# Kernel optimization log

Hardware: AMD Instinct MI355X
Metric: run time of the kernel (lower is better)

Reference implementation:

```python
import jax, jax.numpy as jnp
import numpy as np

EPS = 1e-5
NEG_SLOPE = 0.2


def _minmax(a):
    m = jnp.min(a)
    return (a - m) / (jnp.max(a) - m)


def _bn(x2d, gamma, beta):
    # train-mode BatchNorm1d: stats over axis 0 (biased variance)
    mu = x2d.mean(0)
    var = x2d.var(0)
    return gamma * (x2d - mu) * jax.lax.rsqrt(var + EPS) + beta


def _leaky(a):
    return jnp.where(a >= 0, a, NEG_SLOPE * a)


def setup_inputs() -> dict:
    key = jax.random.key(0)
    ks = jax.random.split(key, 10)
    B, C, N = 256, 1024, 80
    stdv = 1.0 / np.sqrt(C)
    return {
        "x": jax.random.normal(ks[0], (B, C, N), jnp.float32),
        "out1": jax.random.normal(ks[1], (B, N), jnp.float32),
        "adj_param": jax.random.uniform(ks[2], (N, N), jnp.float32),
        "static_weight": jax.random.uniform(ks[3], (C, C), jnp.float32, -stdv, stdv),
        "dynamic_weight": jax.random.uniform(ks[4], (C, C), jnp.float32, -stdv, stdv),
        "conv_global_w": jax.random.normal(ks[5], (C, C), jnp.float32) * 0.02,
        "conv_global_b": jnp.zeros((C,), jnp.float32),
        "conv_co_w": jax.random.normal(ks[6], (N, 2 * C), jnp.float32) * 0.02,
        "conv_co_b": jnp.zeros((N,), jnp.float32),
        "bn_gamma": jnp.ones((C,), jnp.float32),
        "bn_beta": jnp.zeros((C,), jnp.float32),
        "bng_gamma": jnp.ones((C,), jnp.float32),
        "bng_beta": jnp.zeros((C,), jnp.float32),
    }


def reference(x, out1, adj_param, static_weight, dynamic_weight,
              conv_global_w, conv_global_b, conv_co_w, conv_co_b,
              bn_gamma, bn_beta, bng_gamma, bng_beta):
    B, C, N = x.shape

    # ---- static GCN ----
    sadj = _minmax(adj_param)                               # (N,N)
    D = jax.lax.rsqrt(sadj.sum(1))                          # A.sum(1)^-0.5
    adj = D[:, None] * sadj.T * D[None, :]                  # gen_adj, diag matmuls as broadcast
    support = jnp.einsum('bcn,co->bno', x, static_weight)   # (B,N,C)
    h = jnp.einsum('nm,bmo->bno', adj, support)             # (B,N,C)
    h = _bn(h.reshape(-1, C), bn_gamma, bn_beta).reshape(B, N, C)
    out_static = _leaky(h).transpose(0, 2, 1)               # (B,C,N)
    x2 = x + out_static

    # ---- dynamic graph construction ----
    glb = x2.mean(2)                                        # GAP over nodes -> (B,C)
    glb = glb @ conv_global_w.T + conv_global_b             # 1x1 conv
    glb = _leaky(_bn(glb, bng_gamma, bng_beta))             # BN over batch (L=1)
    cat = jnp.concatenate([jnp.broadcast_to(glb[:, :, None], (B, C, N)), x2], axis=1)  # (B,2C,N)
    dadj = jnp.einsum('oc,bcn->bon', conv_co_w, cat) + conv_co_b[None, :, None]        # (B,N,N)
    dadj = _minmax(dadj)

    # ---- adjacency loss ----
    t1 = jnp.einsum('bn,bnm->bm', out1, dadj) / N
    loss = jnp.sum(jnp.linalg.norm(out1 - t1, axis=1))
    loss = loss + jnp.sum(jnp.linalg.norm((dadj - sadj).reshape(B, -1), axis=1))

    # ---- dynamic GCN ----
    Dd = jax.lax.rsqrt(dadj.sum(2))                         # (B,N)
    tadj = Dd[:, :, None] * dadj.transpose(0, 2, 1) * Dd[:, None, :]
    sup = jnp.einsum('bcn,co->bno', x2, dynamic_weight)
    h2 = jnp.einsum('bnm,bmo->bno', tadj, sup)
    h2 = _bn(h2.reshape(-1, C), bn_gamma, bn_beta).reshape(B, N, C).transpose(0, 2, 1)
    h2 = _leaky(h2)                                         # (B,C,N)
    return h2, loss
```

## Files before the change

kernel.cpp:

```cpp
#include <hip/hip_runtime.h>
#include <hip/hip_bf16.h>
#include <math.h>

#define TPB 256

constexpr int   B_  = 256;
constexpr int   C_  = 1024;
constexpr int   N_  = 80;
constexpr int   BNr = B_ * N_;
constexpr int   CN  = C_ * N_;
constexpr long  BCN = (long)B_ * C_ * N_;
constexpr int   NN  = N_ * N_;
constexpr int   BNN = B_ * NN;
constexpr float EPSf = 1e-5f;

typedef __bf16 bf16x8 __attribute__((ext_vector_type(8)));
typedef float  f32x4  __attribute__((ext_vector_type(4)));

__device__ __forceinline__ float leakyf(float v) { return v >= 0.0f ? v : 0.2f * v; }

__device__ __forceinline__ ushort f2bf(float f) {
  __hip_bfloat16 h = __float2bfloat16(f);
  ushort u; __builtin_memcpy(&u, &h, 2); return u;
}
__device__ __forceinline__ float b2f(ushort u) {
  __hip_bfloat16 h; __builtin_memcpy(&h, &u, 2);
  return __bfloat162float(h);
}

#define GLOBAL_AS __attribute__((address_space(1)))
#define LDS_AS    __attribute__((address_space(3)))
__device__ __forceinline__ void load_lds16(const void* g, void* l) {
  __builtin_amdgcn_global_load_lds((const GLOBAL_AS void*)g, (LDS_AS void*)l, 16, 0, 0);
}

__global__ void k_prep_adj(const float* __restrict__ ap, float* __restrict__ sadj,
                           ushort* __restrict__ adj_bf, float* __restrict__ lossa) {
  __shared__ float s[NN];
  __shared__ float red[TPB];
  __shared__ float s_lo, s_hi;
  __shared__ float sD[N_];
  const int t = threadIdx.x;
  float lo = 3.4e38f, hi = -3.4e38f;
  for (int i = t; i < NN; i += TPB) { float v = ap[i]; s[i] = v; lo = fminf(lo, v); hi = fmaxf(hi, v); }
  red[t] = lo; __syncthreads();
  for (int o = 128; o > 0; o >>= 1) { if (t < o) red[t] = fminf(red[t], red[t + o]); __syncthreads(); }
  if (t == 0) s_lo = red[0];
  __syncthreads();
  red[t] = hi; __syncthreads();
  for (int o = 128; o > 0; o >>= 1) { if (t < o) red[t] = fmaxf(red[t], red[t + o]); __syncthreads(); }
  if (t == 0) s_hi = red[0];
  __syncthreads();
  const float inv = 1.0f / (s_hi - s_lo);
  for (int i = t; i < NN; i += TPB) { float v = (s[i] - s_lo) * inv; s[i] = v; sadj[i] = v; }
  __syncthreads();
  if (t < N_) { float sum = 0.f; for (int m = 0; m < N_; ++m) sum += s[t * N_ + m]; sD[t] = rsqrtf(sum); }
  if (t == 0) *lossa = 0.0f;
  __syncthreads();
  for (int i = t; i < N_ * 96; i += TPB) {
    const int n = i / 96, m = i % 96;
    adj_bf[i] = f2bf((m < N_) ? sD[n] * s[m * N_ + n] * sD[m] : 0.0f);
  }
}

__global__ void k_w_bf_t(const float* __restrict__ W, ushort* __restrict__ Wt) {
  __shared__ float s[32][33];
  const int t = threadIdx.x;
  const int tx = t % 32, ty = t / 32;
  const int r0 = blockIdx.y * 32, c0 = blockIdx.x * 32;
#pragma unroll
  for (int k = 0; k < 4; ++k) s[ty + 8 * k][tx] = W[(size_t)(r0 + ty + 8 * k) * C_ + c0 + tx];
  __syncthreads();
#pragma unroll
  for (int k = 0; k < 4; ++k) Wt[(size_t)(c0 + ty + 8 * k) * C_ + r0 + tx] = f2bf(s[tx][ty + 8 * k]);
}

__global__ void k_wco_bf(const float* __restrict__ Wco, ushort* __restrict__ Wco1t,
                         ushort* __restrict__ Wco2t) {
  const int i4 = (blockIdx.x * TPB + threadIdx.x) * 4;
  const int o = i4 >> 11, k = i4 & 2047;
  float4 v = *(const float4*)&Wco[(size_t)o * 2048 + k];
  ushort4 u;
  u.x = f2bf(v.x); u.y = f2bf(v.y); u.z = f2bf(v.z); u.w = f2bf(v.w);
  if (k < C_) *(ushort4*)&Wco1t[(size_t)o * C_ + k] = u;
  else        *(ushort4*)&Wco2t[(size_t)o * C_ + (k - C_)] = u;
}

__global__ void k_cvt_bf(const float* __restrict__ W, ushort* __restrict__ Wb) {
  const long i4 = ((long)blockIdx.x * TPB + threadIdx.x) * 4;
  float4 v = *(const float4*)&W[i4];
  ushort4 u;
  u.x = f2bf(v.x); u.y = f2bf(v.y); u.z = f2bf(v.z); u.w = f2bf(v.w);
  *(ushort4*)&Wb[i4] = u;
}

__global__ void k_zero_go(float* __restrict__ go) {
  const int i = (blockIdx.x * TPB + threadIdx.x) * 4;
  float4 z = make_float4(0.f, 0.f, 0.f, 0.f);
  *(float4*)&go[i] = z;
}

__global__ __launch_bounds__(256) void k_fold_mfma(const float* __restrict__ Xf32,
                                                   const ushort* __restrict__ Xbf,
                                                   const void* __restrict__ adjsrc,
                                                   ushort* __restrict__ outp, int mode,
                                                   const float* __restrict__ dmm) {
  __shared__ __align__(16) ushort sX[128][104];
  __shared__ __align__(16) ushort sAdj[80][104];
  __shared__ float sD[N_];
  const int t = threadIdx.x;
  const int b  = blockIdx.x >> 3;
  const int c0 = (blockIdx.x & 7) * 128;

  if (mode == 0) {
    const ushort* ab = (const ushort*)adjsrc;
    for (int i = t; i < (N_ * 96) / 4; i += TPB) {
      ushort4 v = *(const ushort4*)&ab[i * 4];
      *(ushort4*)&sAdj[(i * 4) / 96][(i * 4) % 96] = v;
    }
    __syncthreads();
  } else {
    float* sF = (float*)&sX[0][0];
    const float* db = (const float*)adjsrc + (size_t)b * NN;
    const float lo = dmm[0], inv = dmm[1];
    for (int i = t; i < NN / 4; i += TPB) {
      float4 v = *(const float4*)&db[i * 4];
      v.x = (v.x - lo) * inv; v.y = (v.y - lo) * inv;
      v.z = (v.z - lo) * inv; v.w = (v.w - lo) * inv;
      *(float4*)&sF[i * 4] = v;
    }
    __syncthreads();
    if (t < N_) { float s = 0.f; for (int m = 0; m < N_; ++m) s += sF[t * N_ + m]; sD[t] = rsqrtf(s); }
    __syncthreads();
    for (int i = t; i < N_ * 96; i += TPB) {
      const int n = i / 96, m = i % 96;
      sAdj[n][m] = f2bf((m < N_) ? sF[m * N_ + n] * sD[n] * sD[m] : 0.0f);
    }
    __syncthreads();
  }

  if (mode == 0) {
    const float* Xb = Xf32 + ((size_t)b * C_ + c0) * N_;
    for (int i = t; i < (128 * N_) / 4; i += TPB) {
      float4 v = *(const float4*)&Xb[i * 4];
      const int r = (i * 4) / N_, m = (i * 4) % N_;
      ushort4 u; u.x = f2bf(v.x); u.y = f2bf(v.y); u.z = f2bf(v.z); u.w = f2bf(v.w);
      *(ushort4*)&sX[r][m] = u;
    }
  } else {
    const ushort* Xb = Xbf + ((size_t)b * C_ + c0) * N_;
    for (int i = t; i < (128 * N_) / 8; i += TPB) {
      const int r = i / 10, m = (i % 10) * 8;
      uint4 v = *(const uint4*)&Xb[(size_t)r * N_ + m];
      *(uint4*)&sX[r][m] = v;
    }
  }
  for (int i = t; i < (128 * 16) / 4; i += TPB) {
    const int r = i / 4, m = 80 + (i % 4) * 4;
    ushort4 z; z.x = 0; z.y = 0; z.z = 0; z.w = 0;
    *(ushort4*)&sX[r][m] = z;
  }
  __syncthreads();

  const int lane = t & 63, wid = t >> 6;
  const int l16 = lane & 15, lq = lane >> 4;
  f32x4 acc[2][5];
#pragma unroll
  for (int i = 0; i < 2; ++i)
#pragma unroll
    for (int j = 0; j < 5; ++j) { f32x4 z = {0.f, 0.f, 0.f, 0.f}; acc[i][j] = z; }
  bf16x8 af[2][3], bfr[5][3];
#pragma unroll
  for (int i = 0; i < 2; ++i)
#pragma unroll
    for (int kk = 0; kk < 3; ++kk)
      af[i][kk] = *(const bf16x8*)&sX[wid * 32 + i * 16 + l16][kk * 32 + lq * 8];
#pragma unroll
  for (int j = 0; j < 5; ++j)
#pragma unroll
    for (int kk = 0; kk < 3; ++kk)
      bfr[j][kk] = *(const bf16x8*)&sAdj[j * 16 + l16][kk * 32 + lq * 8];
#pragma unroll
  for (int i = 0; i < 2; ++i)
#pragma unroll
    for (int j = 0; j < 5; ++j)
#pragma unroll
      for (int kk = 0; kk < 3; ++kk)
        acc[i][j] = __builtin_amdgcn_mfma_f32_16x16x32_bf16(af[i][kk], bfr[j][kk], acc[i][j], 0, 0, 0);

  ushort* ob = outp + (size_t)b * CN;
#pragma unroll
  for (int i = 0; i < 2; ++i) {
    const int c = c0 + wid * 32 + i * 16 + lq * 4;
#pragma unroll
    for (int j = 0; j < 5; ++j) {
      const int n = j * 16 + l16;
      ushort4 u;
      u.x = f2bf(acc[i][j][0]); u.y = f2bf(acc[i][j][1]);
      u.z = f2bf(acc[i][j][2]); u.w = f2bf(acc[i][j][3]);
      *(ushort4*)&ob[(size_t)n * C_ + c] = u;
    }
  }
}

__global__ __launch_bounds__(512, 2) void k_gemm_256(const ushort* __restrict__ A,
                                                     const ushort* __restrict__ Bt,
                                                     void* __restrict__ outp, int out_bf) {
  __shared__ ushort sA[2][256 * 64];
  __shared__ ushort sB[2][256 * 64];
  const int t = threadIdx.x;
  const int lane = t & 63, wid = t >> 6;
  const int wm = wid >> 2, wn = wid & 3;
  const int l16 = lane & 15, lq = lane >> 4;

  const int lin = blockIdx.x;
  const int xcd = lin & 7, bi = lin >> 3;
  const int tm = xcd * 10 + (bi >> 2);
  const int tn = bi & 3;
  const int m0 = tm * 256, o0 = tn * 256;

  const int srow = t >> 3;
  const int sswz = ((t & 7) ^ ((t >> 3) & 7)) * 8;

  f32x4 acc[8][4];
#pragma unroll
  for (int i = 0; i < 8; ++i)
#pragma unroll
    for (int j = 0; j < 4; ++j) { f32x4 z = {0.f, 0.f, 0.f, 0.f}; acc[i][j] = z; }

  bf16x8 afr[4][2], bfr0[2][2], bfr1[2][2];

#define STA(PAR, ROWB, KT) load_lds16(A  + (size_t)(m0 + (ROWB) + srow) * C_ + (KT) * 64 + sswz, \
                                      &sA[PAR][((ROWB) + (wid << 3)) * 64])
#define STB(PAR, ROWB, KT) load_lds16(Bt + (size_t)(o0 + (ROWB) + srow) * C_ + (KT) * 64 + sswz, \
                                      &sB[PAR][((ROWB) + (wid << 3)) * 64])
#define STA_H(PAR, H, KT) { STA(PAR, (H)*128, KT); STA(PAR, (H)*128 + 64, KT); }
#define STB_H(PAR, H, KT) { STB(PAR, (H)*128, KT); STB(PAR, (H)*128 + 64, KT); }

#define RDA(PAR, MH)                                                                      \
  _Pragma("unroll") for (int fi = 0; fi < 4; ++fi) {                                      \
    const int row = ((MH) ? 128 : 0) + wm * 64 + fi * 16 + l16;                           \
    _Pragma("unroll") for (int kk = 0; kk < 2; ++kk)                                      \
      afr[fi][kk] = *(const bf16x8*)&sA[PAR][row * 64 + ((kk * 4 + lq) ^ (l16 & 7)) * 8]; \
  }
#define RDB(PAR, NH, DST)                                                                 \
  _Pragma("unroll") for (int gi = 0; gi < 2; ++gi) {                                      \
    const int row = ((NH) ? 128 : 0) + wn * 32 + gi * 16 + l16;                           \
    _Pragma("unroll") for (int kk = 0; kk < 2; ++kk)                                      \
      DST[gi][kk] = *(const bf16x8*)&sB[PAR][row * 64 + ((kk * 4 + lq) ^ (l16 & 7)) * 8]; \
  }

#define MFMAS(MH, NH, BF)                                                          \
  _Pragma("unroll") for (int kk = 0; kk < 2; ++kk)                                 \
  _Pragma("unroll") for (int fi = 0; fi < 4; ++fi)                                 \
  _Pragma("unroll") for (int gi = 0; gi < 2; ++gi)                                 \
    acc[(MH) * 4 + fi][(NH) * 2 + gi] = __builtin_amdgcn_mfma_f32_16x16x32_bf16(   \
        afr[fi][kk], BF[gi][kk], acc[(MH) * 4 + fi][(NH) * 2 + gi], 0, 0, 0);

#define PHASE(MH, NH, BF, RD, STAGES, VMW)                                         \
  {                                                                                \
    RD                                                                             \
    STAGES                                                                         \
    asm volatile("s_barrier" ::: "memory");                                        \
    asm volatile("s_waitcnt lgkmcnt(0)" ::: "memory");                             \
    __builtin_amdgcn_s_setprio(1);                                                 \
    MFMAS(MH, NH, BF)                                                              \
    __builtin_amdgcn_s_setprio(0);                                                 \
    VMW                                                                            \
    asm volatile("s_barrier" ::: "memory");                                        \
  }

  STA_H(0, 0, 0); STA_H(0, 1, 0); STB_H(0, 0, 0); STB_H(0, 1, 0);
  STA_H(1, 0, 1); STB_H(1, 1, 1);
  asm volatile("s_waitcnt vmcnt(4)" ::: "memory");
  asm volatile("s_barrier" ::: "memory");

  for (int i = 0; i < 7; ++i) {
    const int t1 = 2 * i + 1, t2 = 2 * i + 2, t3 = 2 * i + 3;
    PHASE(0, 0, bfr0, RDA(0, 0) RDB(0, 0, bfr0), { STA_H(1, 1, t1); }, {})
    PHASE(0, 1, bfr1, RDB(0, 1, bfr1),           { STB_H(1, 0, t1); }, {})
    PHASE(1, 1, bfr1, RDA(0, 1),                 { STA_H(0, 0, t2); }, {})
    PHASE(1, 0, bfr0, {},                        { STB_H(0, 1, t2); }, { asm volatile("s_waitcnt vmcnt(4)" ::: "memory"); })
    PHASE(0, 0, bfr0, RDA(1, 0) RDB(1, 0, bfr0), { STA_H(0, 1, t2); }, {})
    PHASE(0, 1, bfr1, RDB(1, 1, bfr1),           { STB_H(0, 0, t2); }, {})
    PHASE(1, 1, bfr1, RDA(1, 1),                 { STA_H(1, 0, t3); }, {})
    PHASE(1, 0, bfr0, {},                        { STB_H(1, 1, t3); }, { asm volatile("s_waitcnt vmcnt(4)" ::: "memory"); })
  }
  PHASE(0, 0, bfr0, RDA(0, 0) RDB(0, 0, bfr0), { STA_H(1, 1, 15); }, {})
  PHASE(0, 1, bfr1, RDB(0, 1, bfr1),           { STB_H(1, 0, 15); }, {})
  PHASE(1, 1, bfr1, RDA(0, 1),                 {}, {})
  PHASE(1, 0, bfr0, {},                        {}, { asm volatile("s_waitcnt vmcnt(0)" ::: "memory"); })
  PHASE(0, 0, bfr0, RDA(1, 0) RDB(1, 0, bfr0), {}, {})
  PHASE(0, 1, bfr1, RDB(1, 1, bfr1),           {}, {})
  PHASE(1, 1, bfr1, RDA(1, 1),                 {}, {})
  PHASE(1, 0, bfr0, {},                        {}, {})

#pragma unroll
  for (int f = 0; f < 8; ++f) {
    const int gmb = (f < 4) ? (wm * 64 + f * 16) : (128 + wm * 64 + (f - 4) * 16);
    const int mg = m0 + gmb + lq * 4;
    const int b  = mg / 80;
    const int n0 = mg - b * 80;
#pragma unroll
    for (int gi = 0; gi < 4; ++gi) {
      const int gnb = (gi < 2) ? (wn * 32 + gi * 16) : (128 + wn * 32 + (gi - 2) * 16);
      const int og = o0 + gnb + l16;
      const size_t off = (size_t)b * CN + (size_t)og * N_ + n0;
      if (out_bf) {
        ushort4 u;
        u.x = f2bf(acc[f][gi][0]); u.y = f2bf(acc[f][gi][1]);
        u.z = f2bf(acc[f][gi][2]); u.w = f2bf(acc[f][gi][3]);
        *(ushort4*)((ushort*)outp + off) = u;
      } else {
        *(f32x4*)((float*)outp + off) = acc[f][gi];
      }
    }
  }
#undef STA
#undef STB
#undef STA_H
#undef STB_H
#undef RDA
#undef RDB
#undef MFMAS
#undef PHASE
}

__global__ __launch_bounds__(256) void k_dadj_mfma(const ushort* __restrict__ A,
                                                   const ushort* __restrict__ Bw,
                                                   const float* __restrict__ go,
                                                   const float* __restrict__ bco,
                                                   float* __restrict__ dadj,
                                                   float* __restrict__ bmin,
                                                   float* __restrict__ bmax) {
  __shared__ ushort smA[128 * 32];
  __shared__ ushort smB[80 * 32];
  const int t = threadIdx.x;
  const int lane = t & 63, wid = t >> 6;
  const int m0 = blockIdx.x * 128;
  const int rto = t >> 2, ch = t & 3;
  const size_t gA0 = (size_t)(m0 + rto) * C_ + (size_t)ch * 8;
  ushort* ldsA = smA + wid * 512;
  const int l16 = lane & 15, lq = lane >> 4;
  const int wrow = wid * 32;
  f32x4 zero = {0.f, 0.f, 0.f, 0.f};
  f32x4 acc[2][5];
#pragma unroll
  for (int i = 0; i < 2; ++i)
#pragma unroll
    for (int j = 0; j < 5; ++j) acc[i][j] = zero;
  for (int k0 = 0; k0 < C_; k0 += 32) {
    load_lds16(A + gA0 + k0,            ldsA);
    load_lds16(A + gA0 + 64 * C_ + k0,  ldsA + 2048);
    {
      const int idx = t;
      uint4 v = *(const uint4*)&Bw[(size_t)(idx >> 2) * C_ + k0 + (idx & 3) * 8];
      *(uint4*)&smB[idx * 8] = v;
      if (t < 64) {
        const int idx2 = 256 + t;
        uint4 v2 = *(const uint4*)&Bw[(size_t)(idx2 >> 2) * C_ + k0 + (idx2 & 3) * 8];
        *(uint4*)&smB[idx2 * 8] = v2;
      }
    }
    __syncthreads();
    bf16x8 af[2], bfr[5];
#pragma unroll
    for (int i = 0; i < 2; ++i) af[i]  = *(const bf16x8*)&smA[(wrow + i * 16 + l16) * 32 + lq * 8];
#pragma unroll
    for (int j = 0; j < 5; ++j) bfr[j] = *(const bf16x8*)&smB[(j * 16 + l16) * 32 + lq * 8];
#pragma unroll
    for (int i = 0; i < 2; ++i)
#pragma unroll
      for (int j = 0; j < 5; ++j)
        acc[i][j] = __builtin_amdgcn_mfma_f32_16x16x32_bf16(af[i], bfr[j], acc[i][j], 0, 0, 0);
    __syncthreads();
  }
  float vlo = 3.4e38f, vhi = -3.4e38f;
#pragma unroll
  for (int i = 0; i < 2; ++i) {
    const int mg = m0 + wrow + i * 16 + lq * 4;
    const int b  = mg / 80;
    const int n0 = mg - b * 80;
    const float* gob = go + b * N_;
#pragma unroll
    for (int j = 0; j < 5; ++j) {
      const int o = j * 16 + l16;
      const float g = gob[o] + bco[o];
      f32x4 v = acc[i][j];
      v[0] += g; v[1] += g; v[2] += g; v[3] += g;
      vlo = fminf(vlo, fminf(fminf(v[0], v[1]), fminf(v[2], v[3])));
      vhi = fmaxf(vhi, fmaxf(fmaxf(v[0], v[1]), fmaxf(v[2], v[3])));
      *(f32x4*)&dadj[(size_t)b * NN + (size_t)o * N_ + n0] = v;
    }
  }
  float* red = (float*)smA;
  red[t] = vlo; red[TPB + t] = vhi;
  __syncthreads();
  for (int o = 128; o > 0; o >>= 1) {
    if (t < o) {
      red[t] = fminf(red[t], red[t + o]);
      red[TPB + t] = fmaxf(red[TPB + t], red[TPB + t + o]);
    }
    __syncthreads();
  }
  if (t == 0) { bmin[blockIdx.x] = red[0]; bmax[blockIdx.x] = red[TPB]; }
}

__global__ __launch_bounds__(256) void k_glb_mfma(const ushort* __restrict__ A,
                                                  const ushort* __restrict__ Bw,
                                                  const float* __restrict__ bias,
                                                  float* __restrict__ outp) {
  __shared__ ushort smA[2][64 * 32];
  __shared__ ushort smB[2][64 * 32];
  const int t = threadIdx.x;
  const int lane = t & 63, wid = t >> 6;
  const int o0 = blockIdx.x * 64, m0 = blockIdx.y * 64;
  const int rto = t >> 2, ch = t & 3;
  const size_t gA0 = (size_t)(m0 + rto) * C_ + (size_t)ch * 8;
  const size_t gB0 = (size_t)(o0 + rto) * C_ + (size_t)ch * 8;
  const int l16 = lane & 15, lq = lane >> 4;
  const int wm = wid & 1, wn = wid >> 1;
  f32x4 zero = {0.f, 0.f, 0.f, 0.f};
  f32x4 acc[2][2];
#pragma unroll
  for (int i = 0; i < 2; ++i)
#pragma unroll
    for (int j = 0; j < 2; ++j) acc[i][j] = zero;
  for (int k0 = 0; k0 < C_; k0 += 64) {
    load_lds16(A  + gA0 + k0,       smA[0] + wid * 512);
    load_lds16(A  + gA0 + k0 + 32,  smA[1] + wid * 512);
    load_lds16(Bw + gB0 + k0,       smB[0] + wid * 512);
    load_lds16(Bw + gB0 + k0 + 32,  smB[1] + wid * 512);
    __syncthreads();
#pragma unroll
    for (int h = 0; h < 2; ++h) {
      bf16x8 af[2], bfr[2];
#pragma unroll
      for (int i = 0; i < 2; ++i) af[i]  = *(const bf16x8*)&smA[h][(wm * 32 + i * 16 + l16) * 32 + lq * 8];
#pragma unroll
      for (int j = 0; j < 2; ++j) bfr[j] = *(const bf16x8*)&smB[h][(wn * 32 + j * 16 + l16) * 32 + lq * 8];
#pragma unroll
      for (int i = 0; i < 2; ++i)
#pragma unroll
        for (int j = 0; j < 2; ++j)
          acc[i][j] = __builtin_amdgcn_mfma_f32_16x16x32_bf16(af[i], bfr[j], acc[i][j], 0, 0, 0);
    }
    __syncthreads();
  }
#pragma unroll
  for (int i = 0; i < 2; ++i) {
    const int mg = m0 + wm * 32 + i * 16 + lq * 4;
#pragma unroll
    for (int j = 0; j < 2; ++j) {
      const int og = o0 + wn * 32 + j * 16 + l16;
      const float bs = bias[og];
      f32x4 v = acc[i][j];
#pragma unroll
      for (int r = 0; r < 4; ++r) outp[(size_t)(mg + r) * C_ + og] = v[r] + bs;
    }
  }
}

__global__ __launch_bounds__(256) void k_go_mfma(const ushort* __restrict__ A,
                                                 const ushort* __restrict__ Bw,
                                                 float* __restrict__ go) {
  __shared__ ushort smA[128 * 32];
  __shared__ ushort smB[80 * 32];
  const int t = threadIdx.x;
  const int lane = t & 63, wid = t >> 6;
  const int kbase = blockIdx.x * 128;
  const int m0 = blockIdx.y * 128;
  const int rto = t >> 2, ch = t & 3;
  const size_t gA0 = (size_t)(m0 + rto) * C_ + (size_t)ch * 8;
  ushort* ldsA = smA + wid * 512;
  const int l16 = lane & 15, lq = lane >> 4;
  const int wrow = wid * 32;
  f32x4 zero = {0.f, 0.f, 0.f, 0.f};
  f32x4 acc[2][5];
#pragma unroll
  for (int i = 0; i < 2; ++i)
#pragma unroll
    for (int j = 0; j < 5; ++j) acc[i][j] = zero;
  for (int kk0 = 0; kk0 < 128; kk0 += 32) {
    const int k0 = kbase + kk0;
    load_lds16(A + gA0 + k0,            ldsA);
    load_lds16(A + gA0 + 64 * C_ + k0,  ldsA + 2048);
    {
      const int idx = t;
      uint4 v = *(const uint4*)&Bw[(size_t)(idx >> 2) * C_ + k0 + (idx & 3) * 8];
      *(uint4*)&smB[idx * 8] = v;
      if (t < 64) {
        const int idx2 = 256 + t;
        uint4 v2 = *(const uint4*)&Bw[(size_t)(idx2 >> 2) * C_ + k0 + (idx2 & 3) * 8];
        *(uint4*)&smB[idx2 * 8] = v2;
      }
    }
    __syncthreads();
    bf16x8 af[2], bfr[5];
#pragma unroll
    for (int i = 0; i < 2; ++i) af[i]  = *(const bf16x8*)&smA[(wrow + i * 16 + l16) * 32 + lq * 8];
#pragma unroll
    for (int j = 0; j < 5; ++j) bfr[j] = *(const bf16x8*)&smB[(j * 16 + l16) * 32 + lq * 8];
#pragma unroll
    for (int i = 0; i < 2; ++i)
#pragma unroll
      for (int j = 0; j < 5; ++j)
        acc[i][j] = __builtin_amdgcn_mfma_f32_16x16x32_bf16(af[i], bfr[j], acc[i][j], 0, 0, 0);
    __syncthreads();
  }
#pragma unroll
  for (int i = 0; i < 2; ++i) {
    const int mg = m0 + wrow + i * 16 + lq * 4;
#pragma unroll
    for (int j = 0; j < 5; ++j) {
      const int o = j * 16 + l16;
#pragma unroll
      for (int r = 0; r < 4; ++r)
        atomicAdd(&go[(size_t)(mg + r) * N_ + o], acc[i][j][r]);
    }
  }
}

__global__ void k_bn_stats_bf(const ushort* __restrict__ X, float* __restrict__ mu, float* __restrict__ rstd) {
  const int c = blockIdx.x, t = threadIdx.x;
  const ushort* base = X + (long)c * N_;
  float s = 0.f, sq = 0.f;
  for (int i4 = t; i4 < BNr / 4; i4 += TPB) {
    const int b = i4 / 20, n0 = (i4 % 20) * 4;
    ushort4 v = *(const ushort4*)&base[(long)b * CN + n0];
    const float f0 = b2f(v.x), f1 = b2f(v.y), f2 = b2f(v.z), f3 = b2f(v.w);
    s += f0 + f1 + f2 + f3;
    sq += f0 * f0 + f1 * f1 + f2 * f2 + f3 * f3;
  }
  __shared__ float rs[TPB], rq[TPB];
  rs[t] = s; rq[t] = sq; __syncthreads();
  for (int o = 128; o > 0; o >>= 1) { if (t < o) { rs[t] += rs[t + o]; rq[t] += rq[t + o]; } __syncthreads(); }
  if (t == 0) {
    const float m = rs[0] / BNr;
    const float var = rq[0] / BNr - m * m;
    mu[c] = m;
    rstd[c] = rsqrtf(var + EPSf);
  }
}

__global__ __launch_bounds__(256) void k_x2_fused(
    const float* __restrict__ x, ushort* __restrict__ hx,
    const float* __restrict__ g, const float* __restrict__ be,
    const float* __restrict__ mu, const float* __restrict__ rstd,
    ushort* __restrict__ x2t, ushort* __restrict__ glb0b) {
  __shared__ float s[64][84];
  __shared__ float pg[64], pm[64], pb[64];
  const int t = threadIdx.x;
  const long row0 = (long)blockIdx.x * 64;
  const int b = (int)(row0 >> 10), c0 = (int)(row0 & 1023);
  if (t < 64) {
    const int c = c0 + t;
    pg[t] = g[c] * rstd[c]; pm[t] = mu[c]; pb[t] = be[c];
  }
  __syncthreads();
  const float* xb = x  + row0 * N_;
  ushort*      hb = hx + row0 * N_;
  for (int i4 = t; i4 < (64 * N_) / 4; i4 += TPB) {
    const int e = i4 * 4, r = e / N_, n = e % N_;
    float4 xv = *(const float4*)&xb[e];
    ushort4 hu = *(const ushort4*)&hb[e];
    const float gm = pg[r], m = pm[r], bb = pb[r];
    float4 o;
    o.x = xv.x + leakyf(gm * (b2f(hu.x) - m) + bb);
    o.y = xv.y + leakyf(gm * (b2f(hu.y) - m) + bb);
    o.z = xv.z + leakyf(gm * (b2f(hu.z) - m) + bb);
    o.w = xv.w + leakyf(gm * (b2f(hu.w) - m) + bb);
    *(float4*)&s[r][n] = o;
    ushort4 ou;
    ou.x = f2bf(o.x); ou.y = f2bf(o.y); ou.z = f2bf(o.z); ou.w = f2bf(o.w);
    *(ushort4*)&hb[e] = ou;
  }
  __syncthreads();
  const int tx = t % 16, ty = t / 16;
  ushort* tb = x2t + (size_t)b * CN + c0 + tx * 4;
#pragma unroll
  for (int u = 0; u < 5; ++u) {
    const int n = ty + 16 * u;
    ushort4 v;
    v.x = f2bf(s[tx * 4 + 0][n]); v.y = f2bf(s[tx * 4 + 1][n]);
    v.z = f2bf(s[tx * 4 + 2][n]); v.w = f2bf(s[tx * 4 + 3][n]);
    *(ushort4*)&tb[(size_t)n * C_] = v;
  }
  {
    const int r = t >> 2, q = t & 3;
    float sacc = 0.f;
    for (int n = q; n < N_; n += 4) sacc += s[r][n];
    sacc += __shfl_down(sacc, 1);
    sacc += __shfl_down(sacc, 2);
    if (q == 0) glb0b[(size_t)b * C_ + c0 + r] = f2bf(sacc * (1.0f / N_));
  }
}

__global__ void k_bng(const float* __restrict__ glb1, const float* __restrict__ gg,
                      const float* __restrict__ gb, ushort* __restrict__ glbf) {
  const int c = blockIdx.x, t = threadIdx.x;
  const float v = glb1[(long)t * C_ + c];
  __shared__ float rs[TPB], rq[TPB];
  rs[t] = v; rq[t] = v * v; __syncthreads();
  for (int o = 128; o > 0; o >>= 1) { if (t < o) { rs[t] += rs[t + o]; rq[t] += rq[t + o]; } __syncthreads(); }
  __shared__ float sm, sr;
  if (t == 0) { const float m = rs[0] / B_; const float var = rq[0] / B_ - m * m; sm = m; sr = rsqrtf(var + EPSf); }
  __syncthreads();
  glbf[(long)t * C_ + c] = f2bf(leakyf(gg[c] * (v - sm) * sr + gb[c]));
}

__global__ void k_minmax2(const float* __restrict__ bmin, const float* __restrict__ bmax, float* __restrict__ dmm) {
  const int t = threadIdx.x;
  float lo = (t < 160) ? bmin[t] : 3.4e38f;
  float hi = (t < 160) ? bmax[t] : -3.4e38f;
  __shared__ float rl[TPB], rh[TPB];
  rl[t] = lo; rh[t] = hi; __syncthreads();
  for (int o = 128; o > 0; o >>= 1) { if (t < o) { rl[t] = fminf(rl[t], rl[t + o]); rh[t] = fmaxf(rh[t], rh[t + o]); } __syncthreads(); }
  if (t == 0) { dmm[0] = rl[0]; dmm[1] = 1.0f / (rh[0] - rl[0]); }
}

__global__ void k_loss(const float* __restrict__ dadj, const float* __restrict__ sadj,
                       const float* __restrict__ out1, float* __restrict__ lossa,
                       const float* __restrict__ dmm) {
  const int b = blockIdx.x, t = threadIdx.x;
  const float* db = dadj + (long)b * NN;
  const float* o1 = out1 + b * N_;
  const float lo = dmm[0], inv = dmm[1];
  float p2 = 0.f;
  for (int i = t; i < NN; i += TPB) { const float d = (db[i] - lo) * inv - sadj[i]; p2 += d * d; }
  float p1 = 0.f;
  if (t < N_) {
    float acc = 0.f;
    for (int n = 0; n < N_; ++n) acc += o1[n] * ((db[n * N_ + t] - lo) * inv);
    const float d = o1[t] - acc * (1.0f / N_);
    p1 = d * d;
  }
  __shared__ float red[TPB];
  __shared__ float s2;
  red[t] = p2; __syncthreads();
  for (int o = 128; o > 0; o >>= 1) { if (t < o) red[t] += red[t + o]; __syncthreads(); }
  if (t == 0) s2 = red[0];
  __syncthreads();
  red[t] = p1; __syncthreads();
  for (int o = 128; o > 0; o >>= 1) { if (t < o) red[t] += red[t + o]; __syncthreads(); }
  if (t == 0) atomicAdd(lossa, sqrtf(s2) + sqrtf(red[0]));
}

__global__ void k_final(const ushort* __restrict__ h2, float* __restrict__ outp,
                        const float* __restrict__ g, const float* __restrict__ be,
                        const float* __restrict__ mu, const float* __restrict__ rstd,
                        const float* __restrict__ lossa) {
  const long i = ((long)blockIdx.x * TPB + threadIdx.x) * 4;
  const int c = (int)((i / N_) % C_);
  ushort4 hu = *(const ushort4*)&h2[i];
  const float gm = g[c] * rstd[c], m = mu[c], bb = be[c];
  float4 v;
  v.x = leakyf(gm * (b2f(hu.x) - m) + bb);
  v.y = leakyf(gm * (b2f(hu.y) - m) + bb);
  v.z = leakyf(gm * (b2f(hu.z) - m) + bb);
  v.w = leakyf(gm * (b2f(hu.w) - m) + bb);
  *(float4*)&outp[i] = v;
  if (blockIdx.x == 0 && threadIdx.x == 0) outp[BCN] = *lossa;
}

extern "C" void kernel_launch(void* const* d_in, const int* in_sizes, int n_in,
                              void* d_out, int out_size, void* d_ws, size_t ws_size,
                              hipStream_t stream) {
  const float* x    = (const float*)d_in[0];
  const float* out1 = (const float*)d_in[1];
  const float* ap   = (const float*)d_in[2];
  const float* Ws   = (const float*)d_in[3];
  const float* Wd   = (const float*)d_in[4];
  const float* Wg   = (const float*)d_in[5];
  const float* bg   = (const float*)d_in[6];
  const float* Wco  = (const float*)d_in[7];
  const float* bco  = (const float*)d_in[8];
  const float* bn_g  = (const float*)d_in[9];
  const float* bn_b  = (const float*)d_in[10];
  const float* bng_g = (const float*)d_in[11];
  const float* bng_b = (const float*)d_in[12];
  float* out = (float*)d_out;

  float* w = (float*)d_ws;
  float* sadj  = w;
  float* dadj  = sadj + NN;
  float* glb0  = dadj + BNN;
  float* glb1  = glb0 + B_ * C_;
  float* glbf  = glb1 + B_ * C_;
  float* go    = glbf + B_ * C_;
  float* mu1   = go + BNr;
  float* rstd1 = mu1 + C_;
  float* mu2   = rstd1 + C_;
  float* rstd2 = mu2 + C_;
  float* bmin  = rstd2 + C_;
  float* bmax  = bmin + 512;
  float* dmm   = bmax + 512;
  float* lossa = dmm + 2;
  ushort* ub   = (ushort*)(((uintptr_t)(lossa + 1) + 255) & ~(uintptr_t)255);
  ushort* xa_bf  = ub;
  ushort* hT_bf  = xa_bf + BCN;
  ushort* Wts    = hT_bf + BCN;
  ushort* Wtd    = Wts + (size_t)C_ * C_;
  ushort* Wco2t  = Wtd + (size_t)C_ * C_;
  ushort* adj_bf = Wco2t + (size_t)N_ * C_;
  ushort* Wg_bf   = (ushort*)dadj;
  ushort* Wco1t   = (ushort*)dadj + (size_t)C_ * C_;
  ushort* glb0_bf = (ushort*)glb0;
  ushort* glbf_bf = (ushort*)glbf;
  ushort* x2t_bf  = xa_bf;

  k_prep_adj<<<1, TPB, 0, stream>>>(ap, sadj, adj_bf, lossa);
  k_w_bf_t<<<dim3(32, 32), TPB, 0, stream>>>(Ws, Wts);
  k_w_bf_t<<<dim3(32, 32), TPB, 0, stream>>>(Wd, Wtd);
  k_wco_bf<<<(N_ * 2 * C_) / (4 * TPB), TPB, 0, stream>>>(Wco, Wco1t, Wco2t);
  k_cvt_bf<<<(C_ * C_) / (4 * TPB), TPB, 0, stream>>>(Wg, Wg_bf);
  k_zero_go<<<BNr / (4 * TPB), TPB, 0, stream>>>(go);

  k_fold_mfma<<<B_ * 8, TPB, 0, stream>>>(x, hT_bf, adj_bf, xa_bf, 0, dmm);
  k_gemm_256<<<320, 512, 0, stream>>>(xa_bf, Wts, hT_bf, 1);
  k_bn_stats_bf<<<C_, TPB, 0, stream>>>(hT_bf, mu1, rstd1);
  k_x2_fused<<<(B_ * C_) / 64, TPB, 0, stream>>>(x, hT_bf, bn_g, bn_b, mu1, rstd1,
                                                 x2t_bf, glb0_bf);

  k_glb_mfma<<<dim3(C_ / 64, B_ / 64), TPB, 0, stream>>>(glb0_bf, Wg_bf, bg, glb1);
  k_bng<<<C_, TPB, 0, stream>>>(glb1, bng_g, bng_b, glbf_bf);
  k_go_mfma<<<dim3(8, B_ / 128), TPB, 0, stream>>>(glbf_bf, Wco1t, go);
  k_dadj_mfma<<<BNr / 128, TPB, 0, stream>>>(x2t_bf, Wco2t, go, bco, dadj, bmin, bmax);
  k_minmax2<<<1, TPB, 0, stream>>>(bmin, bmax, dmm);

  k_loss<<<B_, TPB, 0, stream>>>(dadj, sadj, out1, lossa, dmm);

  k_fold_mfma<<<B_ * 8, TPB, 0, stream>>>(x, hT_bf, dadj, xa_bf, 1, dmm);
  k_gemm_256<<<320, 512, 0, stream>>>(xa_bf, Wtd, hT_bf, 1);
  k_bn_stats_bf<<<C_, TPB, 0, stream>>>(hT_bf, mu2, rstd2);
  k_final<<<(int)(BCN / (4 * TPB)), TPB, 0, stream>>>(hT_bf, out, bn_g, bn_b, mu2, rstd2, lossa);
}
```

Baseline: 534.5 us.

## Fuse BN statistics into GEMM epilogue and merge prep kernels into one launch

Each GEMM block now reduces per-channel sum and sum-of-squares from its fp32 accumulators, combining them in LDS and then with global atomics. This removes the two separate BN-stats kernels that re-read the full bf16 hidden tensor. Consumers derive mean and rstd from these sums inline. The six weight-conversion, zeroing and adjacency-prep kernels are merged into one block-indexed launch, which also zeroes the new stat accumulators. In exchange, stats come from unrounded accumulators, the float atomics make summation order nondeterministic, and reusing the sA LDS buffer for the reduction may race with waves still reading it.

```diff
diff --git a/kernel.cpp b/kernel.cpp
--- a/kernel.cpp
+++ b/kernel.cpp
@@ -34,70 +34,72 @@
   __builtin_amdgcn_global_load_lds((const GLOBAL_AS void*)g, (LDS_AS void*)l, 16, 0, 0);
 }
 
-__global__ void k_prep_adj(const float* __restrict__ ap, float* __restrict__ sadj,
-                           ushort* __restrict__ adj_bf, float* __restrict__ lossa) {
-  __shared__ float s[NN];
+__global__ __launch_bounds__(256) void k_prep_all(
+    const float* __restrict__ Ws, const float* __restrict__ Wd,
+    const float* __restrict__ Wco, const float* __restrict__ Wg,
+    ushort* __restrict__ Wts, ushort* __restrict__ Wtd,
+    ushort* __restrict__ Wco1t, ushort* __restrict__ Wco2t, ushort* __restrict__ Wg_bf,
+    float* __restrict__ zbase,
+    const float* __restrict__ ap, float* __restrict__ sadj,
+    ushort* __restrict__ adj_bf, float* __restrict__ lossa) {
+  __shared__ float sh[NN];
   __shared__ float red[TPB];
+  __shared__ float sD[N_];
   __shared__ float s_lo, s_hi;
-  __shared__ float sD[N_];
   const int t = threadIdx.x;
-  float lo = 3.4e38f, hi = -3.4e38f;
-  for (int i = t; i < NN; i += TPB) { float v = ap[i]; s[i] = v; lo = fminf(lo, v); hi = fmaxf(hi, v); }
-  red[t] = lo; __syncthreads();
-  for (int o = 128; o > 0; o >>= 1) { if (t < o) red[t] = fminf(red[t], red[t + o]); __syncthreads(); }
-  if (t == 0) s_lo = red[0];
-  __syncthreads();
-  red[t] = hi; __syncthreads();
-  for (int o = 128; o > 0; o >>= 1) { if (t < o) red[t] = fmaxf(red[t], red[t + o]); __syncthreads(); }
-  if (t == 0) s_hi = red[0];
-  __syncthreads();
-  const float inv = 1.0f / (s_hi - s_lo);
-  for (int i = t; i < NN; i += TPB) { float v = (s[i] - s_lo) * inv; s[i] = v; sadj[i] = v; }
-  __syncthreads();
-  if (t < N_) { float sum = 0.f; for (int m = 0; m < N_; ++m) sum += s[t * N_ + m]; sD[t] = rsqrtf(sum); }
-  if (t == 0) *lossa = 0.0f;
-  __syncthreads();
-  for (int i = t; i < N_ * 96; i += TPB) {
-    const int n = i / 96, m = i % 96;
-    adj_bf[i] = f2bf((m < N_) ? sD[n] * s[m * N_ + n] * sD[m] : 0.0f);
-  }
-}
-
-__global__ void k_w_bf_t(const float* __restrict__ W, ushort* __restrict__ Wt) {
-  __shared__ float s[32][33];
-  const int t = threadIdx.x;
-  const int tx = t % 32, ty = t / 32;
-  const int r0 = blockIdx.y * 32, c0 = blockIdx.x * 32;
-#pragma unroll
-  for (int k = 0; k < 4; ++k) s[ty + 8 * k][tx] = W[(size_t)(r0 + ty + 8 * k) * C_ + c0 + tx];
-  __syncthreads();
-#pragma unroll
-  for (int k = 0; k < 4; ++k) Wt[(size_t)(c0 + ty + 8 * k) * C_ + r0 + tx] = f2bf(s[tx][ty + 8 * k]);
-}
-
-__global__ void k_wco_bf(const float* __restrict__ Wco, ushort* __restrict__ Wco1t,
-                         ushort* __restrict__ Wco2t) {
-  const int i4 = (blockIdx.x * TPB + threadIdx.x) * 4;
-  const int o = i4 >> 11, k = i4 & 2047;
-  float4 v = *(const float4*)&Wco[(size_t)o * 2048 + k];
-  ushort4 u;
-  u.x = f2bf(v.x); u.y = f2bf(v.y); u.z = f2bf(v.z); u.w = f2bf(v.w);
-  if (k < C_) *(ushort4*)&Wco1t[(size_t)o * C_ + k] = u;
-  else        *(ushort4*)&Wco2t[(size_t)o * C_ + (k - C_)] = u;
-}
-
-__global__ void k_cvt_bf(const float* __restrict__ W, ushort* __restrict__ Wb) {
-  const long i4 = ((long)blockIdx.x * TPB + threadIdx.x) * 4;
-  float4 v = *(const float4*)&W[i4];
-  ushort4 u;
-  u.x = f2bf(v.x); u.y = f2bf(v.y); u.z = f2bf(v.z); u.w = f2bf(v.w);
-  *(ushort4*)&Wb[i4] = u;
-}
-
-__global__ void k_zero_go(float* __restrict__ go) {
-  const int i = (blockIdx.x * TPB + threadIdx.x) * 4;
-  float4 z = make_float4(0.f, 0.f, 0.f, 0.f);
-  *(float4*)&go[i] = z;
+  const int blk = blockIdx.x;
+  if (blk < 2048) {
+    const float* W = (blk < 1024) ? Ws : Wd;
+    ushort* Wt = (blk < 1024) ? Wts : Wtd;
+    const int bb = blk & 1023;
+    const int bx = bb & 31, by = bb >> 5;
+    const int tx = t % 32, ty = t / 32;
+    const int r0 = by * 32, c0 = bx * 32;
+#pragma unroll
+    for (int k = 0; k < 4; ++k) sh[(ty + 8 * k) * 33 + tx] = W[(size_t)(r0 + ty + 8 * k) * C_ + c0 + tx];
+    __syncthreads();
+#pragma unroll
+    for (int k = 0; k < 4; ++k) Wt[(size_t)(c0 + ty + 8 * k) * C_ + r0 + tx] = f2bf(sh[tx * 33 + ty + 8 * k]);
+  } else if (blk < 2208) {
+    const int i4 = ((blk - 2048) * TPB + t) * 4;
+    const int o = i4 >> 11, k = i4 & 2047;
+    float4 v = *(const float4*)&Wco[(size_t)o * 2048 + k];
+    ushort4 u;
+    u.x = f2bf(v.x); u.y = f2bf(v.y); u.z = f2bf(v.z); u.w = f2bf(v.w);
+    if (k < C_) *(ushort4*)&Wco1t[(size_t)o * C_ + k] = u;
+    else        *(ushort4*)&Wco2t[(size_t)o * C_ + (k - C_)] = u;
+  } else if (blk < 3232) {
+    const long i4 = ((long)(blk - 2208) * TPB + t) * 4;
+    float4 v = *(const float4*)&Wg[i4];
+    ushort4 u;
+    u.x = f2bf(v.x); u.y = f2bf(v.y); u.z = f2bf(v.z); u.w = f2bf(v.w);
+    *(ushort4*)&Wg_bf[i4] = u;
+  } else if (blk < 3256) {
+    const int i = ((blk - 3232) * TPB + t) * 4;
+    float4 z = make_float4(0.f, 0.f, 0.f, 0.f);
+    *(float4*)&zbase[i] = z;
+  } else {
+    float lo = 3.4e38f, hi = -3.4e38f;
+    for (int i = t; i < NN; i += TPB) { float v = ap[i]; sh[i] = v; lo = fminf(lo, v); hi = fmaxf(hi, v); }
+    red[t] = lo; __syncthreads();
+    for (int o = 128; o > 0; o >>= 1) { if (t < o) red[t] = fminf(red[t], red[t + o]); __syncthreads(); }
+    if (t == 0) s_lo = red[0];
+    __syncthreads();
+    red[t] = hi; __syncthreads();
+    for (int o = 128; o > 0; o >>= 1) { if (t < o) red[t] = fmaxf(red[t], red[t + o]); __syncthreads(); }
+    if (t == 0) s_hi = red[0];
+    __syncthreads();
+    const float inv = 1.0f / (s_hi - s_lo);
+    for (int i = t; i < NN; i += TPB) { float v = (sh[i] - s_lo) * inv; sh[i] = v; sadj[i] = v; }
+    __syncthreads();
+    if (t < N_) { float sum = 0.f; for (int m = 0; m < N_; ++m) sum += sh[t * N_ + m]; sD[t] = rsqrtf(sum); }
+    if (t == 0) *lossa = 0.0f;
+    __syncthreads();
+    for (int i = t; i < N_ * 96; i += TPB) {
+      const int n = i / 96, m = i % 96;
+      adj_bf[i] = f2bf((m < N_) ? sD[n] * sh[m * N_ + n] * sD[m] : 0.0f);
+    }
+  }
 }
 
 __global__ __launch_bounds__(256) void k_fold_mfma(const float* __restrict__ Xf32,
@@ -205,7 +207,9 @@
 
 __global__ __launch_bounds__(512, 2) void k_gemm_256(const ushort* __restrict__ A,
                                                      const ushort* __restrict__ Bt,
-                                                     void* __restrict__ outp, int out_bf) {
+                                                     void* __restrict__ outp, int out_bf,
+                                                     float* __restrict__ bnsum,
+                                                     float* __restrict__ bnsq) {
   __shared__ ushort sA[2][256 * 64];
   __shared__ ushort sB[2][256 * 64];
   const int t = threadIdx.x;
@@ -314,6 +318,32 @@
       } else {
         *(f32x4*)((float*)outp + off) = acc[f][gi];
       }
+    }
+  }
+
+  {
+    float* redS = (float*)&sA[0][0];
+    float* redQ = redS + 2048;
+    const int slot = wm * 4 + lq;
+#pragma unroll
+    for (int gi = 0; gi < 4; ++gi) {
+      float s = 0.f, q = 0.f;
+#pragma unroll
+      for (int f = 0; f < 8; ++f)
+#pragma unroll
+        for (int r = 0; r < 4; ++r) { const float v = acc[f][gi][r]; s += v; q += v * v; }
+      const int gnb = (gi < 2) ? (wn * 32 + gi * 16) : (128 + wn * 32 + (gi - 2) * 16);
+      const int ol = gnb + l16;
+      redS[ol * 8 + slot] = s;
+      redQ[ol * 8 + slot] = q;
+    }
+    __syncthreads();
+    if (t < 256) {
+      float s = 0.f, q = 0.f;
+#pragma unroll
+      for (int k = 0; k < 8; ++k) { s += redS[t * 8 + k]; q += redQ[t * 8 + k]; }
+      atomicAdd(&bnsum[o0 + t], s);
+      atomicAdd(&bnsq[o0 + t], q);
     }
   }
 #undef STA
@@ -521,32 +551,10 @@
   }
 }
 
-__global__ void k_bn_stats_bf(const ushort* __restrict__ X, float* __restrict__ mu, float* __restrict__ rstd) {
-  const int c = blockIdx.x, t = threadIdx.x;
-  const ushort* base = X + (long)c * N_;
-  float s = 0.f, sq = 0.f;
-  for (int i4 = t; i4 < BNr / 4; i4 += TPB) {
-    const int b = i4 / 20, n0 = (i4 % 20) * 4;
-    ushort4 v = *(const ushort4*)&base[(long)b * CN + n0];
-    const float f0 = b2f(v.x), f1 = b2f(v.y), f2 = b2f(v.z), f3 = b2f(v.w);
-    s += f0 + f1 + f2 + f3;
-    sq += f0 * f0 + f1 * f1 + f2 * f2 + f3 * f3;
-  }
-  __shared__ float rs[TPB], rq[TPB];
-  rs[t] = s; rq[t] = sq; __syncthreads();
-  for (int o = 128; o > 0; o >>= 1) { if (t < o) { rs[t] += rs[t + o]; rq[t] += rq[t + o]; } __syncthreads(); }
-  if (t == 0) {
-    const float m = rs[0] / BNr;
-    const float var = rq[0] / BNr - m * m;
-    mu[c] = m;
-    rstd[c] = rsqrtf(var + EPSf);
-  }
-}
-
 __global__ __launch_bounds__(256) void k_x2_fused(
     const float* __restrict__ x, ushort* __restrict__ hx,
     const float* __restrict__ g, const float* __restrict__ be,
-    const float* __restrict__ mu, const float* __restrict__ rstd,
+    const float* __restrict__ ssum, const float* __restrict__ ssq,
     ushort* __restrict__ x2t, ushort* __restrict__ glb0b) {
   __shared__ float s[64][84];
   __shared__ float pg[64], pm[64], pb[64];
@@ -555,7 +563,10 @@
   const int b = (int)(row0 >> 10), c0 = (int)(row0 & 1023);
   if (t < 64) {
     const int c = c0 + t;
-    pg[t] = g[c] * rstd[c]; pm[t] = mu[c]; pb[t] = be[c];
+    const float mu = ssum[c] * (1.0f / BNr);
+    const float var = ssq[c] * (1.0f / BNr) - mu * mu;
+    const float rstd = rsqrtf(var + EPSf);
+    pg[t] = g[c] * rstd; pm[t] = mu; pb[t] = be[c];
   }
   __syncthreads();
   const float* xb = x  + row0 * N_;
@@ -648,17 +659,19 @@
 
 __global__ void k_final(const ushort* __restrict__ h2, float* __restrict__ outp,
                         const float* __restrict__ g, const float* __restrict__ be,
-                        const float* __restrict__ mu, const float* __restrict__ rstd,
+                        const float* __restrict__ ssum, const float* __restrict__ ssq,
                         const float* __restrict__ lossa) {
   const long i = ((long)blockIdx.x * TPB + threadIdx.x) * 4;
   const int c = (int)((i / N_) % C_);
   ushort4 hu = *(const ushort4*)&h2[i];
-  const float gm = g[c] * rstd[c], m = mu[c], bb = be[c];
+  const float mu = ssum[c] * (1.0f / BNr);
+  const float rstd = rsqrtf(ssq[c] * (1.0f / BNr) - mu * mu + EPSf);
+  const float gm = g[c] * rstd, bb = be[c];
   float4 v;
-  v.x = leakyf(gm * (b2f(hu.x) - m) + bb);
-  v.y = leakyf(gm * (b2f(hu.y) - m) + bb);
-  v.z = leakyf(gm * (b2f(hu.z) - m) + bb);
-  v.w = leakyf(gm * (b2f(hu.w) - m) + bb);
+  v.x = leakyf(gm * (b2f(hu.x) - mu) + bb);
+  v.y = leakyf(gm * (b2f(hu.y) - mu) + bb);
+  v.z = leakyf(gm * (b2f(hu.z) - mu) + bb);
+  v.w = leakyf(gm * (b2f(hu.w) - mu) + bb);
   *(float4*)&outp[i] = v;
   if (blockIdx.x == 0 && threadIdx.x == 0) outp[BCN] = *lossa;
 }
@@ -688,11 +701,11 @@
   float* glb1  = glb0 + B_ * C_;
   float* glbf  = glb1 + B_ * C_;
   float* go    = glbf + B_ * C_;
-  float* mu1   = go + BNr;
-  float* rstd1 = mu1 + C_;
-  float* mu2   = rstd1 + C_;
-  float* rstd2 = mu2 + C_;
-  float* bmin  = rstd2 + C_;
+  float* ssum1 = go + BNr;
+  float* ssq1  = ssum1 + C_;
+  float* ssum2 = ssq1 + C_;
+  float* ssq2  = ssum2 + C_;
+  float* bmin  = ssq2 + C_;
   float* bmax  = bmin + 512;
   float* dmm   = bmax + 512;
   float* lossa = dmm + 2;
@@ -709,17 +722,12 @@
   ushort* glbf_bf = (ushort*)glbf;
   ushort* x2t_bf  = xa_bf;
 
-  k_prep_adj<<<1, TPB, 0, stream>>>(ap, sadj, adj_bf, lossa);
-  k_w_bf_t<<<dim3(32, 32), TPB, 0, stream>>>(Ws, Wts);
-  k_w_bf_t<<<dim3(32, 32), TPB, 0, stream>>>(Wd, Wtd);
-  k_wco_bf<<<(N_ * 2 * C_) / (4 * TPB), TPB, 0, stream>>>(Wco, Wco1t, Wco2t);
-  k_cvt_bf<<<(C_ * C_) / (4 * TPB), TPB, 0, stream>>>(Wg, Wg_bf);
-  k_zero_go<<<BNr / (4 * TPB), TPB, 0, stream>>>(go);
+  k_prep_all<<<3257, TPB, 0, stream>>>(Ws, Wd, Wco, Wg, Wts, Wtd, Wco1t, Wco2t, Wg_bf,
+                                       go, ap, sadj, adj_bf, lossa);
 
   k_fold_mfma<<<B_ * 8, TPB, 0, stream>>>(x, hT_bf, adj_bf, xa_bf, 0, dmm);
-  k_gemm_256<<<320, 512, 0, stream>>>(xa_bf, Wts, hT_bf, 1);
-  k_bn_stats_bf<<<C_, TPB, 0, stream>>>(hT_bf, mu1, rstd1);
-  k_x2_fused<<<(B_ * C_) / 64, TPB, 0, stream>>>(x, hT_bf, bn_g, bn_b, mu1, rstd1,
+  k_gemm_256<<<320, 512, 0, stream>>>(xa_bf, Wts, hT_bf, 1, ssum1, ssq1);
+  k_x2_fused<<<(B_ * C_) / 64, TPB, 0, stream>>>(x, hT_bf, bn_g, bn_b, ssum1, ssq1,
                                                  x2t_bf, glb0_bf);
 
   k_glb_mfma<<<dim3(C_ / 64, B_ / 64), TPB, 0, stream>>>(glb0_bf, Wg_bf, bg, glb1);
@@ -731,7 +739,6 @@
   k_loss<<<B_, TPB, 0, stream>>>(dadj, sadj, out1, lossa, dmm);
 
   k_fold_mfma<<<B_ * 8, TPB, 0, stream>>>(x, hT_bf, dadj, xa_bf, 1, dmm);
-  k_gemm_256<<<320, 512, 0, stream>>>(xa_bf, Wtd, hT_bf, 1);
-  k_bn_stats_bf<<<C_, TPB, 0, stream>>>(hT_bf, mu2, rstd2);
-  k_final<<<(int)(BCN / (4 * TPB)), TPB, 0, stream>>>(hT_bf, out, bn_g, bn_b, mu2, rstd2, lossa);
-}
+  k_gemm_256<<<320, 512, 0, stream>>>(xa_bf, Wtd, hT_bf, 1, ssum2, ssq2);
+  k_final<<<(int)(BCN / (4 * TPB)), TPB, 0, stream>>>(hT_bf, out, bn_g, bn_b, ssum2, ssq2, lossa);
+}
```

Measured after the change: 503.4 us. 1.06x faster.
